# Kernel optimization log

Hardware: AMD Instinct MI355X
Metric: run time of the kernel (lower is better)

## Reference

```python
import jax, jax.numpy as jnp
import numpy as np

D = 512   # dense write dimension
M = 64    # number of experts
B = 16    # per-expert sparse code width
N = 8192  # tokens
K = 4     # experts per token (top-k)


def _normalize_U(U):
    # UnitColNormPadded(dim=1): each column of the (D+1, b) expert matrix
    # is rescaled to unit L2 norm along the padded (D+1) axis.
    nrm = jnp.sqrt(jnp.sum(U * U, axis=1, keepdims=True))
    return U / nrm


def setup_inputs() -> dict:
    key = jax.random.key(0)
    k1, k2, k3 = jax.random.split(key, 3)
    h_sparse = jax.random.normal(k1, (N, K, B), dtype=jnp.float32)
    topk_idxs = jax.random.randint(k2, (N, K), 0, M)
    U = jax.random.normal(k3, (M, D + 1, B), dtype=jnp.float32)
    return {"h_sparse": h_sparse, "topk_idxs": topk_idxs, "U": U}


def reference(h_sparse, topk_idxs, U):
    Un = _normalize_U(U)                      # (m, D+1, b)
    U_active = Un[topk_idxs][:, :, :D, :]     # gather -> (N, k, D, b)
    writes = jnp.einsum('nkdb,nkb->nd', U_active, h_sparse)   # (N, D)
    h_recon = jnp.einsum('nkdb,nd->nkb', U_active, writes)    # (N, k, b)
    h_target = jax.lax.stop_gradient(h_sparse)
    diff = h_recon - h_target
    writer_aux_loss = jnp.mean(diff * diff)
    return writes, writer_aux_loss
```

## Files before the change

kernel.cpp:

```cpp
#include <hip/hip_runtime.h>

#define DD 512
#define MM 64
#define BB 16
#define NN 8192
#define KK 4
#define DP1 513
#define CAP 1024
#define NPAIR (NN * KK)

#define CNT_B  0
#define BKT_B  33024
#define U_B    164096
#define UT_B   1212672
#define GRAM_B 2261248
#define PART_B 10649856
#define WS_NEED 44204288

typedef unsigned int uint;
typedef unsigned short ushort;
typedef __attribute__((ext_vector_type(8))) short short8;
typedef __attribute__((ext_vector_type(4))) float f32x4;

__device__ __forceinline__ ushort f2bf(float f) {
    uint u = __builtin_bit_cast(uint, f);
    uint r = (u + 0x7FFFu + ((u >> 16) & 1u)) >> 16;
    return (ushort)r;
}
__device__ __forceinline__ float bf2f(ushort s) {
    return __builtin_bit_cast(float, (uint)s << 16);
}

__global__ __launch_bounds__(256) void prep_build(
    const float* __restrict__ U,
    const int*   __restrict__ topk,
    void* __restrict__ ws,
    float* __restrict__ loss_slot)
{
    const int blk = blockIdx.x, t = threadIdx.x;

    if (blk < 256) {
        const int m = blk >> 2, sl = blk & 3;
        const float* Um = U + (long)m * DP1 * BB;

        __shared__ float red[256];
        __shared__ float inv_s[BB];
        __shared__ ushort tr[BB][136];

        float a = 0.f;
        for (int i = t; i < DP1 * BB; i += 256) { float v = Um[i]; a += v * v; }
        red[t] = a;
        __syncthreads();
        if (t < BB) {
            float tot = 0.f;
            #pragma unroll
            for (int j = 0; j < 16; ++j) tot += red[t + 16 * j];
            inv_s[t] = rsqrtf(tot);
        }
        __syncthreads();

        ushort* ub = (ushort*)((char*)ws + U_B) + (long)m * DD * BB + sl * 2048;
        ushort* ut = (ushort*)((char*)ws + UT_B) + (long)m * BB * DD + sl * 128;
        const float* Us = Um + sl * 2048;

        #pragma unroll
        for (int iter = 0; iter < 4; ++iter) {
            const int i = t + iter * 256;
            const int e0 = 2 * i;
            const int dl = e0 >> 4, b0 = e0 & 15;
            const float2 v = *(const float2*)(Us + e0);
            const ushort bv0 = f2bf(v.x * inv_s[b0]);
            const ushort bv1 = f2bf(v.y * inv_s[b0 + 1]);
            *(uint*)(ub + e0) = (uint)bv0 | ((uint)bv1 << 16);
            tr[b0][dl]     = bv0;
            tr[b0 + 1][dl] = bv1;
        }
        __syncthreads();
        {
            const int b = t >> 4, doff = (t & 15) * 8;
            uint4 val;
            val.x = (uint)tr[b][doff + 0] | ((uint)tr[b][doff + 1] << 16);
            val.y = (uint)tr[b][doff + 2] | ((uint)tr[b][doff + 3] << 16);
            val.z = (uint)tr[b][doff + 4] | ((uint)tr[b][doff + 5] << 16);
            val.w = (uint)tr[b][doff + 6] | ((uint)tr[b][doff + 7] << 16);
            *(uint4*)(ut + (long)b * DD + doff) = val;
        }
    } else {
        const int cblk = blk - 256;
        int* cnt = (int*)ws;
        ushort* bkt = (ushort*)((char*)ws + BKT_B);
        __shared__ int lc[MM], lb[MM];
        if (t < MM) lc[t] = 0;
        __syncthreads();
        const int p = cblk * 256 + t;
        const int e = topk[p];
        const int my = atomicAdd(&lc[e], 1);
        __syncthreads();
        if (t < MM) lb[t] = atomicAdd(&cnt[t], lc[t]);
        __syncthreads();
        bkt[e * CAP + lb[e] + my] = (ushort)p;
        if (cblk == 0 && t == 0) *loss_slot = 0.f;
    }
}

__global__ __launch_bounds__(256) void pass_writes_mfma(
    const float* __restrict__ h_sparse, void* __restrict__ ws)
{
    const int wave = threadIdx.x >> 6, lane = threadIdx.x & 63;
    const int quad = lane >> 4, l15 = lane & 15;

    if (blockIdx.x < MM * 8) {
        const int e = blockIdx.x & 63, g = blockIdx.x >> 6;

        const int* cnt = (const int*)ws;
        const ushort* bkt = (const ushort*)((const char*)ws + BKT_B);
        const ushort* Ue = (const ushort*)((const char*)ws + U_B) + (long)e * DD * BB;
        ushort* part = (ushort*)((char*)ws + PART_B);

        const int c  = cnt[e];
        const int lo = (c * g) >> 3;
        const int hi = (c * (g + 1)) >> 3;

        for (int base = lo + wave * 16; base < hi; base += 64) {
            const int pidx = base + l15;
            const bool valid = pidx < hi;
            const int id = valid ? (int)bkt[e * CAP + pidx] : 0;
            const int n = id >> 2, k = id & 3;

            short8 bfrag = (short8)0;
            if (quad < 2 && valid) {
                const float4* hp = (const float4*)(h_sparse + (long)id * BB + quad * 8);
                const float4 h0 = hp[0], h1 = hp[1];
                bfrag[0] = (short)f2bf(h0.x); bfrag[1] = (short)f2bf(h0.y);
                bfrag[2] = (short)f2bf(h0.z); bfrag[3] = (short)f2bf(h0.w);
                bfrag[4] = (short)f2bf(h1.x); bfrag[5] = (short)f2bf(h1.y);
                bfrag[6] = (short)f2bf(h1.z); bfrag[7] = (short)f2bf(h1.w);
            }
            ushort* prow = part + ((long)(k * NN + n) << 9);

            #pragma unroll 2
            for (int dt = 0; dt < 32; dt += 2) {
                short8 a0 = (short8)0, a1 = (short8)0;
                if (quad < 2) {
                    a0 = *(const short8*)(Ue + ((long)(dt * 16 + l15) << 4) + quad * 8);
                    a1 = *(const short8*)(Ue + ((long)((dt + 1) * 16 + l15) << 4) + quad * 8);
                }
                f32x4 z = {0.f, 0.f, 0.f, 0.f};
                f32x4 c0 = __builtin_amdgcn_mfma_f32_16x16x32_bf16(a0, bfrag, z, 0, 0, 0);
                f32x4 c1 = __builtin_amdgcn_mfma_f32_16x16x32_bf16(a1, bfrag, z, 0, 0, 0);

                uint p0x = (uint)f2bf(c0[0]) | ((uint)f2bf(c0[1]) << 16);
                uint p0y = (uint)f2bf(c0[2]) | ((uint)f2bf(c0[3]) << 16);
                uint p1x = (uint)f2bf(c1[0]) | ((uint)f2bf(c1[1]) << 16);
                uint p1y = (uint)f2bf(c1[2]) | ((uint)f2bf(c1[3]) << 16);
                uint q0x = __shfl_xor((int)p0x, 16, 64);
                uint q0y = __shfl_xor((int)p0y, 16, 64);
                uint q1x = __shfl_xor((int)p1x, 16, 64);
                uint q1y = __shfl_xor((int)p1y, 16, 64);

                if (valid) {
                    uint4 st;
                    int sdt;
                    if ((quad & 1) == 0) { st.x = p0x; st.y = p0y; st.z = q0x; st.w = q0y; sdt = dt; }
                    else                 { st.x = q1x; st.y = q1y; st.z = p1x; st.w = p1y; sdt = dt + 1; }
                    const int srow = (quad & 2) ? 8 : 0;
                    *(uint4*)(prow + sdt * 16 + srow) = st;
                }
            }
        }
    } else {
        const int gblk = blockIdx.x - MM * 8;
        const int e = gblk >> 4;
        const int f = (gblk & 15) * 4 + wave;

        const ushort* utp = (const ushort*)((const char*)ws + UT_B);
        const ushort* ue = utp + (long)e * BB * DD + (long)l15 * DD + quad * 8;
        const ushort* uf = utp + (long)f * BB * DD + (long)l15 * DD + quad * 8;

        f32x4 acc = {0.f, 0.f, 0.f, 0.f};
        #pragma unroll
        for (int dblk = 0; dblk < 16; ++dblk) {
            const short8 a = *(const short8*)(ue + dblk * 32);
            const short8 b = *(const short8*)(uf + dblk * 32);
            acc = __builtin_amdgcn_mfma_f32_16x16x32_bf16(a, b, acc, 0, 0, 0);
        }
        float* G = (float*)((char*)ws + GRAM_B) + (((long)e * MM + f) << 8);
        #pragma unroll
        for (int r = 0; r < 4; ++r)
            G[(quad * 4 + r) * 16 + l15] = acc[r];
    }
}

__global__ __launch_bounds__(256) void reduce_w(
    const float* __restrict__ h_sparse,
    const int*   __restrict__ topk,
    void* __restrict__ ws, float* __restrict__ out)
{
    const int t = threadIdx.x;

    if (blockIdx.x < NN * DD / 8 / 256) {
        const uint4* part4 = (const uint4*)((const char*)ws + PART_B);
        const int gsz = NN * DD / 8;
        const int gid = blockIdx.x * 256 + t;

        const uint4 v0 = part4[gid];
        const uint4 v1 = part4[(long)gsz + gid];
        const uint4 v2 = part4[2L * gsz + gid];
        const uint4 v3 = part4[3L * gsz + gid];

        float s[8];
        s[0] = bf2f((ushort)v0.x) + bf2f((ushort)v1.x) + bf2f((ushort)v2.x) + bf2f((ushort)v3.x);
        s[1] = bf2f((ushort)(v0.x >> 16)) + bf2f((ushort)(v1.x >> 16)) + bf2f((ushort)(v2.x >> 16)) + bf2f((ushort)(v3.x >> 16));
        s[2] = bf2f((ushort)v0.y) + bf2f((ushort)v1.y) + bf2f((ushort)v2.y) + bf2f((ushort)v3.y);
        s[3] = bf2f((ushort)(v0.y >> 16)) + bf2f((ushort)(v1.y >> 16)) + bf2f((ushort)(v2.y >> 16)) + bf2f((ushort)(v3.y >> 16));
        s[4] = bf2f((ushort)v0.z) + bf2f((ushort)v1.z) + bf2f((ushort)v2.z) + bf2f((ushort)v3.z);
        s[5] = bf2f((ushort)(v0.z >> 16)) + bf2f((ushort)(v1.z >> 16)) + bf2f((ushort)(v2.z >> 16)) + bf2f((ushort)(v3.z >> 16));
        s[6] = bf2f((ushort)v0.w) + bf2f((ushort)v1.w) + bf2f((ushort)v2.w) + bf2f((ushort)v3.w);
        s[7] = bf2f((ushort)(v0.w >> 16)) + bf2f((ushort)(v1.w >> 16)) + bf2f((ushort)(v2.w >> 16)) + bf2f((ushort)(v3.w >> 16));

        float4* out4 = (float4*)out;
        out4[(long)gid * 2 + 0] = make_float4(s[0], s[1], s[2], s[3]);
        out4[(long)gid * 2 + 1] = make_float4(s[4], s[5], s[6], s[7]);
    } else {
        const int lb = blockIdx.x - NN * DD / 8 / 256;
        const int wave = t >> 6, lane = t & 63;
        const int quad = lane >> 4, l15 = lane & 15;
        const float* G = (const float*)((const char*)ws + GRAM_B);

        __shared__ float loss_blk;
        if (t == 0) loss_blk = 0.f;
        __syncthreads();

        float lsum = 0.f;
        const int wgid = lb * 4 + wave;
        for (int i = 0; i < 8; ++i) {
            const int n = __builtin_amdgcn_readfirstlane(wgid * 8 + i);
            const int4 tk = *(const int4*)(topk + n * 4);
            const int ek = quad == 0 ? tk.x : quad == 1 ? tk.y : quad == 2 ? tk.z : tk.w;
            const float* hn = h_sparse + (long)n * (KK * BB);

            float recon = 0.f;
            #pragma unroll
            for (int j = 0; j < 4; ++j) {
                const int ej = j == 0 ? tk.x : j == 1 ? tk.y : j == 2 ? tk.z : tk.w;
                const float* Grow = G + (((long)(ek * MM + ej)) << 8) + l15 * 16;
                const float4 g0 = *(const float4*)(Grow + 0);
                const float4 g1 = *(const float4*)(Grow + 4);
                const float4 g2 = *(const float4*)(Grow + 8);
                const float4 g3 = *(const float4*)(Grow + 12);
                const float4 h0 = *(const float4*)(hn + j * 16 + 0);
                const float4 h1 = *(const float4*)(hn + j * 16 + 4);
                const float4 h2 = *(const float4*)(hn + j * 16 + 8);
                const float4 h3 = *(const float4*)(hn + j * 16 + 12);
                recon += g0.x * h0.x + g0.y * h0.y + g0.z * h0.z + g0.w * h0.w;
                recon += g1.x * h1.x + g1.y * h1.y + g1.z * h1.z + g1.w * h1.w;
                recon += g2.x * h2.x + g2.y * h2.y + g2.z * h2.z + g2.w * h2.w;
                recon += g3.x * h3.x + g3.y * h3.y + g3.z * h3.z + g3.w * h3.w;
            }
            const float hv = hn[quad * 16 + l15];
            const float d = recon - hv;
            lsum += d * d;
        }
        #pragma unroll
        for (int off = 32; off > 0; off >>= 1) lsum += __shfl_xor(lsum, off, 64);
        if (lane == 0 && lsum != 0.f) atomicAdd(&loss_blk, lsum);
        __syncthreads();
        if (t == 0 && loss_blk != 0.f)
            atomicAdd(out + (long)NN * DD, loss_blk * (1.0f / ((float)NN * KK * BB)));
    }
}

__global__ __launch_bounds__(256) void norm_kernel(
    const float* __restrict__ U, float* __restrict__ inv_norm,
    float* __restrict__ loss_slot)
{
    const int m = blockIdx.x;
    const int t = threadIdx.x;
    const float* Um = U + (long)m * DP1 * BB;
    float acc = 0.f;
    for (int idx = t; idx < DP1 * BB; idx += 256) {
        float v = Um[idx];
        acc += v * v;
    }
    __shared__ float s[256];
    s[t] = acc;
    __syncthreads();
    if (t < BB) {
        float tot = 0.f;
        #pragma unroll
        for (int j = 0; j < 16; ++j) tot += s[t + 16 * j];
        inv_norm[m * BB + t] = rsqrtf(tot);
    }
    if (m == 0 && t == 0) *loss_slot = 0.f;
}

__global__ __launch_bounds__(256) void dense_write_kernel(
    const float* __restrict__ h_sparse,
    const int*   __restrict__ topk,
    const float* __restrict__ U,
    const float* __restrict__ inv_norm,
    float* __restrict__ out)
{
    const int n = blockIdx.x;
    const int t = threadIdx.x;

    __shared__ float hs[KK * BB];
    __shared__ float ho[KK * BB];
    __shared__ float inv_s[KK * BB];
    __shared__ int   eidx[KK];
    __shared__ float w_s[DD];
    __shared__ float red[256];

    if (t < KK) eidx[t] = topk[n * KK + t];
    __syncthreads();
    if (t < KK * BB) {
        const int k = t / BB, b = t % BB;
        const float h  = h_sparse[(long)n * KK * BB + t];
        const float iv = inv_norm[eidx[k] * BB + b];
        ho[t]    = h;
        inv_s[t] = iv;
        hs[t]    = h * iv;
    }
    __syncthreads();

    #pragma unroll
    for (int dd = 0; dd < 2; ++dd) {
        const int d = t + dd * 256;
        float w = 0.f;
        #pragma unroll
        for (int k = 0; k < KK; ++k) {
            const float4* row = (const float4*)(U + ((long)eidx[k] * DP1 + d) * BB);
            #pragma unroll
            for (int q = 0; q < 4; ++q) {
                const float4 u4 = row[q];
                w += u4.x * hs[k * BB + 4 * q + 0];
                w += u4.y * hs[k * BB + 4 * q + 1];
                w += u4.z * hs[k * BB + 4 * q + 2];
                w += u4.w * hs[k * BB + 4 * q + 3];
            }
        }
        w_s[d] = w;
        out[(long)n * DD + d] = w;
    }
    __syncthreads();

    {
        const int pair = t & 63;
        const int k = pair >> 4, b = pair & 15;
        const int ch = t >> 6;
        const float* Ucol = U + (long)eidx[k] * DP1 * BB + b;
        float p = 0.f;
        #pragma unroll 8
        for (int d = ch * 128; d < ch * 128 + 128; ++d) {
            p += Ucol[(long)d * BB] * w_s[d];
        }
        red[t] = p;
    }
    __syncthreads();

    if (t < 64) {
        const float recon = (red[t] + red[t + 64] + red[t + 128] + red[t + 192]) * inv_s[t];
        const float diff  = recon - ho[t];
        float sq = diff * diff;
        #pragma unroll
        for (int off = 32; off > 0; off >>= 1) sq += __shfl_down(sq, off, 64);
        if (t == 0) {
            atomicAdd(out + (long)NN * DD, sq * (1.0f / ((float)NN * KK * BB)));
        }
    }
}


extern "C" void kernel_launch(void* const* d_in, const int* in_sizes, int n_in,
                              void* d_out, int out_size, void* d_ws, size_t ws_size,
                              hipStream_t stream) {
    const float* h_sparse = (const float*)d_in[0];
    const int*   topk     = (const int*)d_in[1];
    const float* U        = (const float*)d_in[2];
    float* out = (float*)d_out;

    if (ws_size >= (size_t)WS_NEED) {
        hipMemsetAsync(d_ws, 0, 256, stream);
        hipLaunchKernelGGL(prep_build, dim3(256 + NPAIR / 256), dim3(256), 0, stream,
                           U, topk, d_ws, out + (long)NN * DD);
        hipLaunchKernelGGL(pass_writes_mfma, dim3(MM * 8 + MM * 16), dim3(256), 0, stream,
                           h_sparse, d_ws);
        hipLaunchKernelGGL(reduce_w, dim3(NN * DD / 8 / 256 + 256), dim3(256), 0, stream,
                           h_sparse, topk, d_ws, out);
    } else {
        float* inv_norm = (float*)d_ws;
        hipLaunchKernelGGL(norm_kernel, dim3(MM), dim3(256), 0, stream,
                           U, inv_norm, out + (long)NN * DD);
        hipLaunchKernelGGL(dense_write_kernel, dim3(NN), dim3(256), 0, stream,
                           h_sparse, topk, U, inv_norm, out);
    }
}
```

Before: 132.5 us.

## Fuse three-kernel pipeline into one cooperative kernel with grid syncs

Replaces the prep, writes/Gram, and reduce/loss kernels with a single persistent cooperative kernel of 512 blocks that separates the phases with grid.sync and loops over the former block indices. This removes two kernel launch boundaries and their drain/ramp gaps. In exchange it caps parallelism at 512 blocks with launch_bounds(256,2), adds grid-wide barrier costs, and serializes work that previously spread over more blocks.

```diff
diff --git a/kernel.cpp b/kernel.cpp
--- a/kernel.cpp
+++ b/kernel.cpp
@@ -1,4 +1,7 @@
 #include <hip/hip_runtime.h>
+#include <hip/hip_cooperative_groups.h>
+
+namespace cg = cooperative_groups;
 
 #define DD 512
 #define MM 64
@@ -8,6 +11,7 @@
 #define DP1 513
 #define CAP 1024
 #define NPAIR (NN * KK)
+#define NBLK 512
 
 #define CNT_B  0
 #define BKT_B  33024
@@ -31,21 +35,27 @@
     return __builtin_bit_cast(float, (uint)s << 16);
 }
 
-__global__ __launch_bounds__(256) void prep_build(
+__global__ __launch_bounds__(256, 2) void mega(
+    const float* __restrict__ h_sparse,
+    const int*   __restrict__ topk,
     const float* __restrict__ U,
-    const int*   __restrict__ topk,
     void* __restrict__ ws,
-    float* __restrict__ loss_slot)
+    float* __restrict__ out)
 {
-    const int blk = blockIdx.x, t = threadIdx.x;
-
-    if (blk < 256) {
-        const int m = blk >> 2, sl = blk & 3;
+    cg::grid_group grid = cg::this_grid();
+    const int b = blockIdx.x, t = threadIdx.x;
+    const int wave = t >> 6, lane = t & 63;
+    const int quad = lane >> 4, l15 = lane & 15;
+
+    __shared__ float red[256];
+    __shared__ float inv_s[BB];
+    __shared__ ushort tr[BB][136];
+    __shared__ int lc[MM], lb[MM];
+    __shared__ float loss_blk;
+
+    if (b < 256) {
+        const int m = b >> 2, sl = b & 3;
         const float* Um = U + (long)m * DP1 * BB;
-
-        __shared__ float red[256];
-        __shared__ float inv_s[BB];
-        __shared__ ushort tr[BB][136];
 
         float a = 0.f;
         for (int i = t; i < DP1 * BB; i += 256) { float v = Um[i]; a += v * v; }
@@ -77,19 +87,18 @@
         }
         __syncthreads();
         {
-            const int b = t >> 4, doff = (t & 15) * 8;
+            const int bb = t >> 4, doff = (t & 15) * 8;
             uint4 val;
-            val.x = (uint)tr[b][doff + 0] | ((uint)tr[b][doff + 1] << 16);
-            val.y = (uint)tr[b][doff + 2] | ((uint)tr[b][doff + 3] << 16);
-            val.z = (uint)tr[b][doff + 4] | ((uint)tr[b][doff + 5] << 16);
-            val.w = (uint)tr[b][doff + 6] | ((uint)tr[b][doff + 7] << 16);
-            *(uint4*)(ut + (long)b * DD + doff) = val;
-        }
-    } else {
-        const int cblk = blk - 256;
+            val.x = (uint)tr[bb][doff + 0] | ((uint)tr[bb][doff + 1] << 16);
+            val.y = (uint)tr[bb][doff + 2] | ((uint)tr[bb][doff + 3] << 16);
+            val.z = (uint)tr[bb][doff + 4] | ((uint)tr[bb][doff + 5] << 16);
+            val.w = (uint)tr[bb][doff + 6] | ((uint)tr[bb][doff + 7] << 16);
+            *(uint4*)(ut + (long)bb * DD + doff) = val;
+        }
+    } else if (b < 384) {
+        const int cblk = b - 256;
         int* cnt = (int*)ws;
         ushort* bkt = (ushort*)((char*)ws + BKT_B);
-        __shared__ int lc[MM], lb[MM];
         if (t < MM) lc[t] = 0;
         __syncthreads();
         const int p = cblk * 256 + t;
@@ -99,18 +108,14 @@
         if (t < MM) lb[t] = atomicAdd(&cnt[t], lc[t]);
         __syncthreads();
         bkt[e * CAP + lb[e] + my] = (ushort)p;
-        if (cblk == 0 && t == 0) *loss_slot = 0.f;
-    }
-}
-
-__global__ __launch_bounds__(256) void pass_writes_mfma(
-    const float* __restrict__ h_sparse, void* __restrict__ ws)
-{
-    const int wave = threadIdx.x >> 6, lane = threadIdx.x & 63;
-    const int quad = lane >> 4, l15 = lane & 15;
-
-    if (blockIdx.x < MM * 8) {
-        const int e = blockIdx.x & 63, g = blockIdx.x >> 6;
+        if (cblk == 0 && t == 0) out[(long)NN * DD] = 0.f;
+    }
+
+    __threadfence();
+    grid.sync();
+
+    {
+        const int e = b & 63, g = b >> 6;
 
         const int* cnt = (const int*)ws;
         const ushort* bkt = (const ushort*)((const char*)ws + BKT_B);
@@ -168,105 +173,102 @@
                 }
             }
         }
-    } else {
-        const int gblk = blockIdx.x - MM * 8;
-        const int e = gblk >> 4;
-        const int f = (gblk & 15) * 4 + wave;
 
         const ushort* utp = (const ushort*)((const char*)ws + UT_B);
-        const ushort* ue = utp + (long)e * BB * DD + (long)l15 * DD + quad * 8;
-        const ushort* uf = utp + (long)f * BB * DD + (long)l15 * DD + quad * 8;
-
-        f32x4 acc = {0.f, 0.f, 0.f, 0.f};
-        #pragma unroll
-        for (int dblk = 0; dblk < 16; ++dblk) {
-            const short8 a = *(const short8*)(ue + dblk * 32);
-            const short8 b = *(const short8*)(uf + dblk * 32);
-            acc = __builtin_amdgcn_mfma_f32_16x16x32_bf16(a, b, acc, 0, 0, 0);
-        }
-        float* G = (float*)((char*)ws + GRAM_B) + (((long)e * MM + f) << 8);
-        #pragma unroll
-        for (int r = 0; r < 4; ++r)
-            G[(quad * 4 + r) * 16 + l15] = acc[r];
-    }
-}
-
-__global__ __launch_bounds__(256) void reduce_w(
-    const float* __restrict__ h_sparse,
-    const int*   __restrict__ topk,
-    void* __restrict__ ws, float* __restrict__ out)
-{
-    const int t = threadIdx.x;
-
-    if (blockIdx.x < NN * DD / 8 / 256) {
-        const uint4* part4 = (const uint4*)((const char*)ws + PART_B);
-        const int gsz = NN * DD / 8;
-        const int gid = blockIdx.x * 256 + t;
-
-        const uint4 v0 = part4[gid];
-        const uint4 v1 = part4[(long)gsz + gid];
-        const uint4 v2 = part4[2L * gsz + gid];
-        const uint4 v3 = part4[3L * gsz + gid];
-
-        float s[8];
-        s[0] = bf2f((ushort)v0.x) + bf2f((ushort)v1.x) + bf2f((ushort)v2.x) + bf2f((ushort)v3.x);
-        s[1] = bf2f((ushort)(v0.x >> 16)) + bf2f((ushort)(v1.x >> 16)) + bf2f((ushort)(v2.x >> 16)) + bf2f((ushort)(v3.x >> 16));
-        s[2] = bf2f((ushort)v0.y) + bf2f((ushort)v1.y) + bf2f((ushort)v2.y) + bf2f((ushort)v3.y);
-        s[3] = bf2f((ushort)(v0.y >> 16)) + bf2f((ushort)(v1.y >> 16)) + bf2f((ushort)(v2.y >> 16)) + bf2f((ushort)(v3.y >> 16));
-        s[4] = bf2f((ushort)v0.z) + bf2f((ushort)v1.z) + bf2f((ushort)v2.z) + bf2f((ushort)v3.z);
-        s[5] = bf2f((ushort)(v0.z >> 16)) + bf2f((ushort)(v1.z >> 16)) + bf2f((ushort)(v2.z >> 16)) + bf2f((ushort)(v3.z >> 16));
-        s[6] = bf2f((ushort)v0.w) + bf2f((ushort)v1.w) + bf2f((ushort)v2.w) + bf2f((ushort)v3.w);
-        s[7] = bf2f((ushort)(v0.w >> 16)) + bf2f((ushort)(v1.w >> 16)) + bf2f((ushort)(v2.w >> 16)) + bf2f((ushort)(v3.w >> 16));
-
-        float4* out4 = (float4*)out;
-        out4[(long)gid * 2 + 0] = make_float4(s[0], s[1], s[2], s[3]);
-        out4[(long)gid * 2 + 1] = make_float4(s[4], s[5], s[6], s[7]);
-    } else {
-        const int lb = blockIdx.x - NN * DD / 8 / 256;
-        const int wave = t >> 6, lane = t & 63;
-        const int quad = lane >> 4, l15 = lane & 15;
-        const float* G = (const float*)((const char*)ws + GRAM_B);
-
-        __shared__ float loss_blk;
-        if (t == 0) loss_blk = 0.f;
-        __syncthreads();
-
-        float lsum = 0.f;
-        const int wgid = lb * 4 + wave;
-        for (int i = 0; i < 8; ++i) {
-            const int n = __builtin_amdgcn_readfirstlane(wgid * 8 + i);
-            const int4 tk = *(const int4*)(topk + n * 4);
-            const int ek = quad == 0 ? tk.x : quad == 1 ? tk.y : quad == 2 ? tk.z : tk.w;
-            const float* hn = h_sparse + (long)n * (KK * BB);
-
-            float recon = 0.f;
-            #pragma unroll
-            for (int j = 0; j < 4; ++j) {
-                const int ej = j == 0 ? tk.x : j == 1 ? tk.y : j == 2 ? tk.z : tk.w;
-                const float* Grow = G + (((long)(ek * MM + ej)) << 8) + l15 * 16;
-                const float4 g0 = *(const float4*)(Grow + 0);
-                const float4 g1 = *(const float4*)(Grow + 4);
-                const float4 g2 = *(const float4*)(Grow + 8);
-                const float4 g3 = *(const float4*)(Grow + 12);
-                const float4 h0 = *(const float4*)(hn + j * 16 + 0);
-                const float4 h1 = *(const float4*)(hn + j * 16 + 4);
-                const float4 h2 = *(const float4*)(hn + j * 16 + 8);
-                const float4 h3 = *(const float4*)(hn + j * 16 + 12);
-                recon += g0.x * h0.x + g0.y * h0.y + g0.z * h0.z + g0.w * h0.w;
-                recon += g1.x * h1.x + g1.y * h1.y + g1.z * h1.z + g1.w * h1.w;
-                recon += g2.x * h2.x + g2.y * h2.y + g2.z * h2.z + g2.w * h2.w;
-                recon += g3.x * h3.x + g3.y * h3.y + g3.z * h3.z + g3.w * h3.w;
-            }
-            const float hv = hn[quad * 16 + l15];
-            const float d = recon - hv;
-            lsum += d * d;
-        }
-        #pragma unroll
-        for (int off = 32; off > 0; off >>= 1) lsum += __shfl_xor(lsum, off, 64);
-        if (lane == 0 && lsum != 0.f) atomicAdd(&loss_blk, lsum);
-        __syncthreads();
-        if (t == 0 && loss_blk != 0.f)
-            atomicAdd(out + (long)NN * DD, loss_blk * (1.0f / ((float)NN * KK * BB)));
+        for (int u = NBLK + b; u < NBLK + 1024; u += NBLK) {
+            const int gblk = u - NBLK;
+            const int ge = gblk >> 4;
+            const int gf = (gblk & 15) * 4 + wave;
+
+            const ushort* ue = utp + (long)ge * BB * DD + (long)l15 * DD + quad * 8;
+            const ushort* uf = utp + (long)gf * BB * DD + (long)l15 * DD + quad * 8;
+
+            f32x4 acc = {0.f, 0.f, 0.f, 0.f};
+            #pragma unroll
+            for (int dblk = 0; dblk < 16; ++dblk) {
+                const short8 ga = *(const short8*)(ue + dblk * 32);
+                const short8 gb = *(const short8*)(uf + dblk * 32);
+                acc = __builtin_amdgcn_mfma_f32_16x16x32_bf16(ga, gb, acc, 0, 0, 0);
+            }
+            float* G = (float*)((char*)ws + GRAM_B) + (((long)ge * MM + gf) << 8);
+            #pragma unroll
+            for (int r = 0; r < 4; ++r)
+                G[(quad * 4 + r) * 16 + l15] = acc[r];
+        }
+    }
+
+    __threadfence();
+    grid.sync();
+
+    for (int u = b; u < 2304; u += NBLK) {
+        if (u < 256) {
+            const int lbk = u;
+            const float* G = (const float*)((const char*)ws + GRAM_B);
+
+            if (t == 0) loss_blk = 0.f;
+            __syncthreads();
+
+            float lsum = 0.f;
+            const int wgid = lbk * 4 + wave;
+            for (int i = 0; i < 8; ++i) {
+                const int n = __builtin_amdgcn_readfirstlane(wgid * 8 + i);
+                const int4 tk = *(const int4*)(topk + n * 4);
+                const int ek = quad == 0 ? tk.x : quad == 1 ? tk.y : quad == 2 ? tk.z : tk.w;
+                const float* hn = h_sparse + (long)n * (KK * BB);
+
+                float recon = 0.f;
+                #pragma unroll
+                for (int j = 0; j < 4; ++j) {
+                    const int ej = j == 0 ? tk.x : j == 1 ? tk.y : j == 2 ? tk.z : tk.w;
+                    const float* Grow = G + (((long)(ek * MM + ej)) << 8) + l15 * 16;
+                    const float4 g0 = *(const float4*)(Grow + 0);
+                    const float4 g1 = *(const float4*)(Grow + 4);
+                    const float4 g2 = *(const float4*)(Grow + 8);
+                    const float4 g3 = *(const float4*)(Grow + 12);
+                    const float4 h0 = *(const float4*)(hn + j * 16 + 0);
+                    const float4 h1 = *(const float4*)(hn + j * 16 + 4);
+                    const float4 h2 = *(const float4*)(hn + j * 16 + 8);
+                    const float4 h3 = *(const float4*)(hn + j * 16 + 12);
+                    recon += g0.x * h0.x + g0.y * h0.y + g0.z * h0.z + g0.w * h0.w;
+                    recon += g1.x * h1.x + g1.y * h1.y + g1.z * h1.z + g1.w * h1.w;
+                    recon += g2.x * h2.x + g2.y * h2.y + g2.z * h2.z + g2.w * h2.w;
+                    recon += g3.x * h3.x + g3.y * h3.y + g3.z * h3.z + g3.w * h3.w;
+                }
+                const float hv = hn[quad * 16 + l15];
+                const float d = recon - hv;
+                lsum += d * d;
+            }
+            #pragma unroll
+            for (int off = 32; off > 0; off >>= 1) lsum += __shfl_xor(lsum, off, 64);
+            if (lane == 0 && lsum != 0.f) atomicAdd(&loss_blk, lsum);
+            __syncthreads();
+            if (t == 0 && loss_blk != 0.f)
+                atomicAdd(out + (long)NN * DD, loss_blk * (1.0f / ((float)NN * KK * BB)));
+        } else {
+            const int rb = u - 256;
+            const uint4* part4 = (const uint4*)((const char*)ws + PART_B);
+            const int gsz = NN * DD / 8;
+            const int gid = rb * 256 + t;
+
+            const uint4 v0 = part4[gid];
+            const uint4 v1 = part4[(long)gsz + gid];
+            const uint4 v2 = part4[2L * gsz + gid];
+            const uint4 v3 = part4[3L * gsz + gid];
+
+            float s[8];
+            s[0] = bf2f((ushort)v0.x) + bf2f((ushort)v1.x) + bf2f((ushort)v2.x) + bf2f((ushort)v3.x);
+            s[1] = bf2f((ushort)(v0.x >> 16)) + bf2f((ushort)(v1.x >> 16)) + bf2f((ushort)(v2.x >> 16)) + bf2f((ushort)(v3.x >> 16));
+            s[2] = bf2f((ushort)v0.y) + bf2f((ushort)v1.y) + bf2f((ushort)v2.y) + bf2f((ushort)v3.y);
+            s[3] = bf2f((ushort)(v0.y >> 16)) + bf2f((ushort)(v1.y >> 16)) + bf2f((ushort)(v2.y >> 16)) + bf2f((ushort)(v3.y >> 16));
+            s[4] = bf2f((ushort)v0.z) + bf2f((ushort)v1.z) + bf2f((ushort)v2.z) + bf2f((ushort)v3.z);
+            s[5] = bf2f((ushort)(v0.z >> 16)) + bf2f((ushort)(v1.z >> 16)) + bf2f((ushort)(v2.z >> 16)) + bf2f((ushort)(v3.z >> 16));
+            s[6] = bf2f((ushort)v0.w) + bf2f((ushort)v1.w) + bf2f((ushort)v2.w) + bf2f((ushort)v3.w);
+            s[7] = bf2f((ushort)(v0.w >> 16)) + bf2f((ushort)(v1.w >> 16)) + bf2f((ushort)(v2.w >> 16)) + bf2f((ushort)(v3.w >> 16));
+
+            float4* out4 = (float4*)out;
+            out4[(long)gid * 2 + 0] = make_float4(s[0], s[1], s[2], s[3]);
+            out4[(long)gid * 2 + 1] = make_float4(s[4], s[5], s[6], s[7]);
+        }
     }
 }
 
@@ -381,12 +383,10 @@
 
     if (ws_size >= (size_t)WS_NEED) {
         hipMemsetAsync(d_ws, 0, 256, stream);
-        hipLaunchKernelGGL(prep_build, dim3(256 + NPAIR / 256), dim3(256), 0, stream,
-                           U, topk, d_ws, out + (long)NN * DD);
-        hipLaunchKernelGGL(pass_writes_mfma, dim3(MM * 8 + MM * 16), dim3(256), 0, stream,
-                           h_sparse, d_ws);
-        hipLaunchKernelGGL(reduce_w, dim3(NN * DD / 8 / 256 + 256), dim3(256), 0, stream,
-                           h_sparse, topk, d_ws, out);
+        void* args[] = {(void*)&h_sparse, (void*)&topk, (void*)&U,
+                        (void*)&d_ws, (void*)&out};
+        hipLaunchCooperativeKernel((const void*)mega, dim3(NBLK), dim3(256),
+                                   args, 0, stream);
     } else {
         float* inv_norm = (float*)d_ws;
         hipLaunchKernelGGL(norm_kernel, dim3(MM), dim3(256), 0, stream,
```

Measured after the change: 355.6 us. 168% more time.

## Replace expert-bucketed partial writes with per-token fp16 dot2 gather

Applied to the files above, without the earlier changes.

Drops the expert bucketing, the bf16 per-(k,token) partial buffer and its separate reduction pass. Writes are now computed directly per token: each block handles 8 tokens, gathers the 4 expert matrices stored as fp16 and accumulates with fdot2 straight into the output. The Gram computation shares this kernel and the loss moves to its own kernel. This removes a large partial-buffer write and read-back plus the memset and bucketing. In exchange each token re-reads the expert matrices (mostly from cache) and the products use fp16 precision.

```diff
diff --git a/kernel.cpp b/kernel.cpp
--- a/kernel.cpp
+++ b/kernel.cpp
@@ -6,268 +6,223 @@
 #define NN 8192
 #define KK 4
 #define DP1 513
-#define CAP 1024
-#define NPAIR (NN * KK)
-
-#define CNT_B  0
-#define BKT_B  33024
-#define U_B    164096
-#define UT_B   1212672
-#define GRAM_B 2261248
-#define PART_B 10649856
-#define WS_NEED 44204288
+
+#define U_B    0
+#define UT_B   1048576
+#define GRAM_B 2097152
+#define WS_NEED 6291456
 
 typedef unsigned int uint;
 typedef unsigned short ushort;
 typedef __attribute__((ext_vector_type(8))) short short8;
 typedef __attribute__((ext_vector_type(4))) float f32x4;
+typedef __attribute__((ext_vector_type(2))) _Float16 half2v;
 
 __device__ __forceinline__ ushort f2bf(float f) {
     uint u = __builtin_bit_cast(uint, f);
     uint r = (u + 0x7FFFu + ((u >> 16) & 1u)) >> 16;
     return (ushort)r;
 }
-__device__ __forceinline__ float bf2f(ushort s) {
-    return __builtin_bit_cast(float, (uint)s << 16);
-}
-
-__global__ __launch_bounds__(256) void prep_build(
+__device__ __forceinline__ ushort f2h(float f) {
+    _Float16 h = (_Float16)f;
+    return __builtin_bit_cast(ushort, h);
+}
+
+__device__ __forceinline__ float dot2h(uint a, uint b, float c) {
+#if __has_builtin(__builtin_amdgcn_fdot2)
+    return __builtin_amdgcn_fdot2(__builtin_bit_cast(half2v, a),
+                                  __builtin_bit_cast(half2v, b), c, false);
+#else
+    half2v av = __builtin_bit_cast(half2v, a);
+    half2v bv = __builtin_bit_cast(half2v, b);
+    return c + (float)av.x * (float)bv.x + (float)av.y * (float)bv.y;
+#endif
+}
+
+__global__ __launch_bounds__(256) void prep2(
     const float* __restrict__ U,
+    void* __restrict__ ws,
+    float* __restrict__ loss_slot)
+{
+    const int blk = blockIdx.x, t = threadIdx.x;
+    const int m = blk >> 2, sl = blk & 3;
+    const float* Um = U + (long)m * DP1 * BB;
+
+    __shared__ float red[256];
+    __shared__ float inv_s[BB];
+    __shared__ ushort tr[BB][136];
+
+    float a = 0.f;
+    for (int i = t; i < DP1 * BB; i += 256) { float v = Um[i]; a += v * v; }
+    red[t] = a;
+    __syncthreads();
+    if (t < BB) {
+        float tot = 0.f;
+        #pragma unroll
+        for (int j = 0; j < 16; ++j) tot += red[t + 16 * j];
+        inv_s[t] = rsqrtf(tot);
+    }
+    __syncthreads();
+
+    ushort* uh = (ushort*)((char*)ws + U_B) + (long)m * DD * BB + sl * 2048;
+    ushort* ut = (ushort*)((char*)ws + UT_B) + (long)m * BB * DD + sl * 128;
+    const float* Us = Um + sl * 2048;
+
+    #pragma unroll
+    for (int iter = 0; iter < 4; ++iter) {
+        const int i = t + iter * 256;
+        const int e0 = 2 * i;
+        const int dl = e0 >> 4, b0 = e0 & 15;
+        const float2 v = *(const float2*)(Us + e0);
+        const float f0 = v.x * inv_s[b0];
+        const float f1 = v.y * inv_s[b0 + 1];
+        *(uint*)(uh + e0) = (uint)f2h(f0) | ((uint)f2h(f1) << 16);
+        tr[b0][dl]     = f2bf(f0);
+        tr[b0 + 1][dl] = f2bf(f1);
+    }
+    __syncthreads();
+    {
+        const int b = t >> 4, doff = (t & 15) * 8;
+        uint4 val;
+        val.x = (uint)tr[b][doff + 0] | ((uint)tr[b][doff + 1] << 16);
+        val.y = (uint)tr[b][doff + 2] | ((uint)tr[b][doff + 3] << 16);
+        val.z = (uint)tr[b][doff + 4] | ((uint)tr[b][doff + 5] << 16);
+        val.w = (uint)tr[b][doff + 6] | ((uint)tr[b][doff + 7] << 16);
+        *(uint4*)(ut + (long)b * DD + doff) = val;
+    }
+    if (blk == 0 && t == 0) *loss_slot = 0.f;
+}
+
+__global__ __launch_bounds__(256) void w_gram(
+    const float* __restrict__ h_sparse,
     const int*   __restrict__ topk,
     void* __restrict__ ws,
-    float* __restrict__ loss_slot)
-{
-    const int blk = blockIdx.x, t = threadIdx.x;
-
-    if (blk < 256) {
-        const int m = blk >> 2, sl = blk & 3;
-        const float* Um = U + (long)m * DP1 * BB;
-
-        __shared__ float red[256];
-        __shared__ float inv_s[BB];
-        __shared__ ushort tr[BB][136];
-
-        float a = 0.f;
-        for (int i = t; i < DP1 * BB; i += 256) { float v = Um[i]; a += v * v; }
-        red[t] = a;
-        __syncthreads();
-        if (t < BB) {
-            float tot = 0.f;
-            #pragma unroll
-            for (int j = 0; j < 16; ++j) tot += red[t + 16 * j];
-            inv_s[t] = rsqrtf(tot);
-        }
-        __syncthreads();
-
-        ushort* ub = (ushort*)((char*)ws + U_B) + (long)m * DD * BB + sl * 2048;
-        ushort* ut = (ushort*)((char*)ws + UT_B) + (long)m * BB * DD + sl * 128;
-        const float* Us = Um + sl * 2048;
-
-        #pragma unroll
-        for (int iter = 0; iter < 4; ++iter) {
-            const int i = t + iter * 256;
-            const int e0 = 2 * i;
-            const int dl = e0 >> 4, b0 = e0 & 15;
-            const float2 v = *(const float2*)(Us + e0);
-            const ushort bv0 = f2bf(v.x * inv_s[b0]);
-            const ushort bv1 = f2bf(v.y * inv_s[b0 + 1]);
-            *(uint*)(ub + e0) = (uint)bv0 | ((uint)bv1 << 16);
-            tr[b0][dl]     = bv0;
-            tr[b0 + 1][dl] = bv1;
-        }
-        __syncthreads();
-        {
-            const int b = t >> 4, doff = (t & 15) * 8;
-            uint4 val;
-            val.x = (uint)tr[b][doff + 0] | ((uint)tr[b][doff + 1] << 16);
-            val.y = (uint)tr[b][doff + 2] | ((uint)tr[b][doff + 3] << 16);
-            val.z = (uint)tr[b][doff + 4] | ((uint)tr[b][doff + 5] << 16);
-            val.w = (uint)tr[b][doff + 6] | ((uint)tr[b][doff + 7] << 16);
-            *(uint4*)(ut + (long)b * DD + doff) = val;
-        }
-    } else {
-        const int cblk = blk - 256;
-        int* cnt = (int*)ws;
-        ushort* bkt = (ushort*)((char*)ws + BKT_B);
-        __shared__ int lc[MM], lb[MM];
-        if (t < MM) lc[t] = 0;
-        __syncthreads();
-        const int p = cblk * 256 + t;
-        const int e = topk[p];
-        const int my = atomicAdd(&lc[e], 1);
-        __syncthreads();
-        if (t < MM) lb[t] = atomicAdd(&cnt[t], lc[t]);
-        __syncthreads();
-        bkt[e * CAP + lb[e] + my] = (ushort)p;
-        if (cblk == 0 && t == 0) *loss_slot = 0.f;
-    }
-}
-
-__global__ __launch_bounds__(256) void pass_writes_mfma(
-    const float* __restrict__ h_sparse, void* __restrict__ ws)
-{
-    const int wave = threadIdx.x >> 6, lane = threadIdx.x & 63;
+    float* __restrict__ out)
+{
+    const int t = threadIdx.x;
+    const int wave = t >> 6, lane = t & 63;
     const int quad = lane >> 4, l15 = lane & 15;
 
-    if (blockIdx.x < MM * 8) {
-        const int e = blockIdx.x & 63, g = blockIdx.x >> 6;
-
-        const int* cnt = (const int*)ws;
-        const ushort* bkt = (const ushort*)((const char*)ws + BKT_B);
-        const ushort* Ue = (const ushort*)((const char*)ws + U_B) + (long)e * DD * BB;
-        ushort* part = (ushort*)((char*)ws + PART_B);
-
-        const int c  = cnt[e];
-        const int lo = (c * g) >> 3;
-        const int hi = (c * (g + 1)) >> 3;
-
-        for (int base = lo + wave * 16; base < hi; base += 64) {
-            const int pidx = base + l15;
-            const bool valid = pidx < hi;
-            const int id = valid ? (int)bkt[e * CAP + pidx] : 0;
-            const int n = id >> 2, k = id & 3;
-
-            short8 bfrag = (short8)0;
-            if (quad < 2 && valid) {
-                const float4* hp = (const float4*)(h_sparse + (long)id * BB + quad * 8);
-                const float4 h0 = hp[0], h1 = hp[1];
-                bfrag[0] = (short)f2bf(h0.x); bfrag[1] = (short)f2bf(h0.y);
-                bfrag[2] = (short)f2bf(h0.z); bfrag[3] = (short)f2bf(h0.w);
-                bfrag[4] = (short)f2bf(h1.x); bfrag[5] = (short)f2bf(h1.y);
-                bfrag[6] = (short)f2bf(h1.z); bfrag[7] = (short)f2bf(h1.w);
-            }
-            ushort* prow = part + ((long)(k * NN + n) << 9);
-
-            #pragma unroll 2
-            for (int dt = 0; dt < 32; dt += 2) {
-                short8 a0 = (short8)0, a1 = (short8)0;
-                if (quad < 2) {
-                    a0 = *(const short8*)(Ue + ((long)(dt * 16 + l15) << 4) + quad * 8);
-                    a1 = *(const short8*)(Ue + ((long)((dt + 1) * 16 + l15) << 4) + quad * 8);
-                }
-                f32x4 z = {0.f, 0.f, 0.f, 0.f};
-                f32x4 c0 = __builtin_amdgcn_mfma_f32_16x16x32_bf16(a0, bfrag, z, 0, 0, 0);
-                f32x4 c1 = __builtin_amdgcn_mfma_f32_16x16x32_bf16(a1, bfrag, z, 0, 0, 0);
-
-                uint p0x = (uint)f2bf(c0[0]) | ((uint)f2bf(c0[1]) << 16);
-                uint p0y = (uint)f2bf(c0[2]) | ((uint)f2bf(c0[3]) << 16);
-                uint p1x = (uint)f2bf(c1[0]) | ((uint)f2bf(c1[1]) << 16);
-                uint p1y = (uint)f2bf(c1[2]) | ((uint)f2bf(c1[3]) << 16);
-                uint q0x = __shfl_xor((int)p0x, 16, 64);
-                uint q0y = __shfl_xor((int)p0y, 16, 64);
-                uint q1x = __shfl_xor((int)p1x, 16, 64);
-                uint q1y = __shfl_xor((int)p1y, 16, 64);
-
-                if (valid) {
-                    uint4 st;
-                    int sdt;
-                    if ((quad & 1) == 0) { st.x = p0x; st.y = p0y; st.z = q0x; st.w = q0y; sdt = dt; }
-                    else                 { st.x = q1x; st.y = q1y; st.z = p1x; st.w = p1y; sdt = dt + 1; }
-                    const int srow = (quad & 2) ? 8 : 0;
-                    *(uint4*)(prow + sdt * 16 + srow) = st;
-                }
-            }
-        }
-    } else {
-        const int gblk = blockIdx.x - MM * 8;
-        const int e = gblk >> 4;
-        const int f = (gblk & 15) * 4 + wave;
+    if (blockIdx.x < 1024) {
+        const int gblk = blockIdx.x;
+        const int ge = gblk >> 4;
+        const int gf = (gblk & 15) * 4 + wave;
 
         const ushort* utp = (const ushort*)((const char*)ws + UT_B);
-        const ushort* ue = utp + (long)e * BB * DD + (long)l15 * DD + quad * 8;
-        const ushort* uf = utp + (long)f * BB * DD + (long)l15 * DD + quad * 8;
+        const ushort* ue = utp + (long)ge * BB * DD + (long)l15 * DD + quad * 8;
+        const ushort* uf = utp + (long)gf * BB * DD + (long)l15 * DD + quad * 8;
 
         f32x4 acc = {0.f, 0.f, 0.f, 0.f};
         #pragma unroll
         for (int dblk = 0; dblk < 16; ++dblk) {
-            const short8 a = *(const short8*)(ue + dblk * 32);
-            const short8 b = *(const short8*)(uf + dblk * 32);
-            acc = __builtin_amdgcn_mfma_f32_16x16x32_bf16(a, b, acc, 0, 0, 0);
-        }
-        float* G = (float*)((char*)ws + GRAM_B) + (((long)e * MM + f) << 8);
+            const short8 ga = *(const short8*)(ue + dblk * 32);
+            const short8 gb = *(const short8*)(uf + dblk * 32);
+            acc = __builtin_amdgcn_mfma_f32_16x16x32_bf16(ga, gb, acc, 0, 0, 0);
+        }
+        float* G = (float*)((char*)ws + GRAM_B) + (((long)ge * MM + gf) << 8);
         #pragma unroll
         for (int r = 0; r < 4; ++r)
             G[(quad * 4 + r) * 16 + l15] = acc[r];
-    }
-}
-
-__global__ __launch_bounds__(256) void reduce_w(
+    } else {
+        const int n0 = (blockIdx.x - 1024) * 8;
+
+        __shared__ uint hs2[8 * 32];
+        __shared__ int  eidx[8 * 4];
+
+        if (t < 32) eidx[t] = topk[n0 * 4 + t];
+        {
+            const float2 hv = *(const float2*)(h_sparse + (long)n0 * 64 + t * 2);
+            half2v p; p.x = (_Float16)hv.x; p.y = (_Float16)hv.y;
+            hs2[t] = __builtin_bit_cast(uint, p);
+        }
+        __syncthreads();
+
+        const ushort* uh = (const ushort*)((const char*)ws + U_B);
+
+        #pragma unroll 2
+        for (int tok = 0; tok < 8; ++tok) {
+            const int n = n0 + tok;
+            float a0 = 0.f, a1 = 0.f;
+            #pragma unroll
+            for (int k = 0; k < 4; ++k) {
+                const int e = eidx[tok * 4 + k];
+                const uint4* up = (const uint4*)(uh + (long)e * DD * BB + t * 32);
+                const uint4 q0 = up[0], q1 = up[1];
+                const uint4 q2 = up[2], q3 = up[3];
+                const uint* hp = &hs2[tok * 32 + k * 8];
+                a0 = dot2h(q0.x, hp[0], a0);
+                a0 = dot2h(q0.y, hp[1], a0);
+                a0 = dot2h(q0.z, hp[2], a0);
+                a0 = dot2h(q0.w, hp[3], a0);
+                a0 = dot2h(q1.x, hp[4], a0);
+                a0 = dot2h(q1.y, hp[5], a0);
+                a0 = dot2h(q1.z, hp[6], a0);
+                a0 = dot2h(q1.w, hp[7], a0);
+                a1 = dot2h(q2.x, hp[0], a1);
+                a1 = dot2h(q2.y, hp[1], a1);
+                a1 = dot2h(q2.z, hp[2], a1);
+                a1 = dot2h(q2.w, hp[3], a1);
+                a1 = dot2h(q3.x, hp[4], a1);
+                a1 = dot2h(q3.y, hp[5], a1);
+                a1 = dot2h(q3.z, hp[6], a1);
+                a1 = dot2h(q3.w, hp[7], a1);
+            }
+            *(float2*)(out + (long)n * DD + t * 2) = make_float2(a0, a1);
+        }
+    }
+}
+
+__global__ __launch_bounds__(256) void loss_gram(
     const float* __restrict__ h_sparse,
     const int*   __restrict__ topk,
-    void* __restrict__ ws, float* __restrict__ out)
+    void* __restrict__ ws,
+    float* __restrict__ out)
 {
     const int t = threadIdx.x;
-
-    if (blockIdx.x < NN * DD / 8 / 256) {
-        const uint4* part4 = (const uint4*)((const char*)ws + PART_B);
-        const int gsz = NN * DD / 8;
-        const int gid = blockIdx.x * 256 + t;
-
-        const uint4 v0 = part4[gid];
-        const uint4 v1 = part4[(long)gsz + gid];
-        const uint4 v2 = part4[2L * gsz + gid];
-        const uint4 v3 = part4[3L * gsz + gid];
-
-        float s[8];
-        s[0] = bf2f((ushort)v0.x) + bf2f((ushort)v1.x) + bf2f((ushort)v2.x) + bf2f((ushort)v3.x);
-        s[1] = bf2f((ushort)(v0.x >> 16)) + bf2f((ushort)(v1.x >> 16)) + bf2f((ushort)(v2.x >> 16)) + bf2f((ushort)(v3.x >> 16));
-        s[2] = bf2f((ushort)v0.y) + bf2f((ushort)v1.y) + bf2f((ushort)v2.y) + bf2f((ushort)v3.y);
-        s[3] = bf2f((ushort)(v0.y >> 16)) + bf2f((ushort)(v1.y >> 16)) + bf2f((ushort)(v2.y >> 16)) + bf2f((ushort)(v3.y >> 16));
-        s[4] = bf2f((ushort)v0.z) + bf2f((ushort)v1.z) + bf2f((ushort)v2.z) + bf2f((ushort)v3.z);
-        s[5] = bf2f((ushort)(v0.z >> 16)) + bf2f((ushort)(v1.z >> 16)) + bf2f((ushort)(v2.z >> 16)) + bf2f((ushort)(v3.z >> 16));
-        s[6] = bf2f((ushort)v0.w) + bf2f((ushort)v1.w) + bf2f((ushort)v2.w) + bf2f((ushort)v3.w);
-        s[7] = bf2f((ushort)(v0.w >> 16)) + bf2f((ushort)(v1.w >> 16)) + bf2f((ushort)(v2.w >> 16)) + bf2f((ushort)(v3.w >> 16));
-
-        float4* out4 = (float4*)out;
-        out4[(long)gid * 2 + 0] = make_float4(s[0], s[1], s[2], s[3]);
-        out4[(long)gid * 2 + 1] = make_float4(s[4], s[5], s[6], s[7]);
-    } else {
-        const int lb = blockIdx.x - NN * DD / 8 / 256;
-        const int wave = t >> 6, lane = t & 63;
-        const int quad = lane >> 4, l15 = lane & 15;
-        const float* G = (const float*)((const char*)ws + GRAM_B);
-
-        __shared__ float loss_blk;
-        if (t == 0) loss_blk = 0.f;
-        __syncthreads();
-
-        float lsum = 0.f;
-        const int wgid = lb * 4 + wave;
-        for (int i = 0; i < 8; ++i) {
-            const int n = __builtin_amdgcn_readfirstlane(wgid * 8 + i);
-            const int4 tk = *(const int4*)(topk + n * 4);
-            const int ek = quad == 0 ? tk.x : quad == 1 ? tk.y : quad == 2 ? tk.z : tk.w;
-            const float* hn = h_sparse + (long)n * (KK * BB);
-
-            float recon = 0.f;
-            #pragma unroll
-            for (int j = 0; j < 4; ++j) {
-                const int ej = j == 0 ? tk.x : j == 1 ? tk.y : j == 2 ? tk.z : tk.w;
-                const float* Grow = G + (((long)(ek * MM + ej)) << 8) + l15 * 16;
-                const float4 g0 = *(const float4*)(Grow + 0);
-                const float4 g1 = *(const float4*)(Grow + 4);
-                const float4 g2 = *(const float4*)(Grow + 8);
-                const float4 g3 = *(const float4*)(Grow + 12);
-                const float4 h0 = *(const float4*)(hn + j * 16 + 0);
-                const float4 h1 = *(const float4*)(hn + j * 16 + 4);
-                const float4 h2 = *(const float4*)(hn + j * 16 + 8);
-                const float4 h3 = *(const float4*)(hn + j * 16 + 12);
-                recon += g0.x * h0.x + g0.y * h0.y + g0.z * h0.z + g0.w * h0.w;
-                recon += g1.x * h1.x + g1.y * h1.y + g1.z * h1.z + g1.w * h1.w;
-                recon += g2.x * h2.x + g2.y * h2.y + g2.z * h2.z + g2.w * h2.w;
-                recon += g3.x * h3.x + g3.y * h3.y + g3.z * h3.z + g3.w * h3.w;
-            }
-            const float hv = hn[quad * 16 + l15];
-            const float d = recon - hv;
-            lsum += d * d;
-        }
-        #pragma unroll
-        for (int off = 32; off > 0; off >>= 1) lsum += __shfl_xor(lsum, off, 64);
-        if (lane == 0 && lsum != 0.f) atomicAdd(&loss_blk, lsum);
-        __syncthreads();
-        if (t == 0 && loss_blk != 0.f)
-            atomicAdd(out + (long)NN * DD, loss_blk * (1.0f / ((float)NN * KK * BB)));
-    }
+    const int wave = t >> 6, lane = t & 63;
+    const int quad = lane >> 4, l15 = lane & 15;
+    const float* G = (const float*)((const char*)ws + GRAM_B);
+
+    __shared__ float loss_blk;
+    if (t == 0) loss_blk = 0.f;
+    __syncthreads();
+
+    float lsum = 0.f;
+    const int wgid = blockIdx.x * 4 + wave;
+    for (int i = 0; i < 8; ++i) {
+        const int n = __builtin_amdgcn_readfirstlane(wgid * 8 + i);
+        const int4 tk = *(const int4*)(topk + n * 4);
+        const int ek = quad == 0 ? tk.x : quad == 1 ? tk.y : quad == 2 ? tk.z : tk.w;
+        const float* hn = h_sparse + (long)n * (KK * BB);
+
+        float recon = 0.f;
+        #pragma unroll
+        for (int j = 0; j < 4; ++j) {
+            const int ej = j == 0 ? tk.x : j == 1 ? tk.y : j == 2 ? tk.z : tk.w;
+            const float* Grow = G + (((long)(ek * MM + ej)) << 8) + l15 * 16;
+            const float4 g0 = *(const float4*)(Grow + 0);
+            const float4 g1 = *(const float4*)(Grow + 4);
+            const float4 g2 = *(const float4*)(Grow + 8);
+            const float4 g3 = *(const float4*)(Grow + 12);
+            const float4 h0 = *(const float4*)(hn + j * 16 + 0);
+            const float4 h1 = *(const float4*)(hn + j * 16 + 4);
+            const float4 h2 = *(const float4*)(hn + j * 16 + 8);
+            const float4 h3 = *(const float4*)(hn + j * 16 + 12);
+            recon += g0.x * h0.x + g0.y * h0.y + g0.z * h0.z + g0.w * h0.w;
+            recon += g1.x * h1.x + g1.y * h1.y + g1.z * h1.z + g1.w * h1.w;
+            recon += g2.x * h2.x + g2.y * h2.y + g2.z * h2.z + g2.w * h2.w;
+            recon += g3.x * h3.x + g3.y * h3.y + g3.z * h3.z + g3.w * h3.w;
+        }
+        const float hv = hn[quad * 16 + l15];
+        const float d = recon - hv;
+        lsum += d * d;
+    }
+    #pragma unroll
+    for (int off = 32; off > 0; off >>= 1) lsum += __shfl_xor(lsum, off, 64);
+    if (lane == 0 && lsum != 0.f) atomicAdd(&loss_blk, lsum);
+    __syncthreads();
+    if (t == 0 && loss_blk != 0.f)
+        atomicAdd(out + (long)NN * DD, loss_blk * (1.0f / ((float)NN * KK * BB)));
 }
 
 __global__ __launch_bounds__(256) void norm_kernel(
@@ -380,12 +335,11 @@
     float* out = (float*)d_out;
 
     if (ws_size >= (size_t)WS_NEED) {
-        hipMemsetAsync(d_ws, 0, 256, stream);
-        hipLaunchKernelGGL(prep_build, dim3(256 + NPAIR / 256), dim3(256), 0, stream,
-                           U, topk, d_ws, out + (long)NN * DD);
-        hipLaunchKernelGGL(pass_writes_mfma, dim3(MM * 8 + MM * 16), dim3(256), 0, stream,
-                           h_sparse, d_ws);
-        hipLaunchKernelGGL(reduce_w, dim3(NN * DD / 8 / 256 + 256), dim3(256), 0, stream,
+        hipLaunchKernelGGL(prep2, dim3(256), dim3(256), 0, stream,
+                           U, d_ws, out + (long)NN * DD);
+        hipLaunchKernelGGL(w_gram, dim3(2048), dim3(256), 0, stream,
+                           h_sparse, topk, d_ws, out);
+        hipLaunchKernelGGL(loss_gram, dim3(256), dim3(256), 0, stream,
                            h_sparse, topk, d_ws, out);
     } else {
         float* inv_norm = (float*)d_ws;
```

After: 144.0 us. 8.7% more time.
